# Kernel tuning notes

Hardware: AMD Instinct MI355X
Metric: run time of the kernel (lower is better)

The kernel has to match this reference:

```python
import jax, jax.numpy as jnp
import numpy as np

PAD_IDX = 1  # word2vec key_to_index['<PAD>'] / padding_idx in the original
VOCAB, EMBED, HIDDEN, SEQ = 100000, 300, 512, 1024


def setup_inputs() -> dict:
    key = jax.random.key(0)
    k = jax.random.split(key, 8)
    s = 1.0 / np.sqrt(HIDDEN)  # PyTorch LSTM init scale
    return {
        "input_seq": jax.random.randint(k[0], (1, SEQ), 0, VOCAB, dtype=jnp.int64)
                     if jax.config.jax_enable_x64 else
                     jax.random.randint(k[0], (1, SEQ), 0, VOCAB, dtype=jnp.int32),
        "h0": jnp.zeros((1, 1, HIDDEN), jnp.float32),
        "c0": jnp.zeros((1, 1, HIDDEN), jnp.float32),
        "emb": jax.random.normal(k[1], (VOCAB, EMBED), jnp.float32),  # frozen word2vec table
        "W_ih": jax.random.uniform(k[2], (4 * HIDDEN, EMBED), jnp.float32, -s, s),
        "W_hh": jax.random.uniform(k[3], (4 * HIDDEN, HIDDEN), jnp.float32, -s, s),
        "b_ih": jax.random.uniform(k[4], (4 * HIDDEN,), jnp.float32, -s, s),
        "b_hh": jax.random.uniform(k[5], (4 * HIDDEN,), jnp.float32, -s, s),
    }


def _lstm_scan(xs, is_pad, h, c, W_ih, W_hh, b_ih, b_hh):
    # xs: [S, E]; PAD steps leave (h, c, out) untouched, matching the `continue`.
    x_gates = xs @ W_ih.T + b_ih  # [S, 4H] -- hoist input projection out of the scan
    H = h.shape[-1]

    def step(carry, inp):
        h, c, out = carry
        xg, pad = inp
        g = xg + h @ W_hh.T + b_hh                 # [4H], PyTorch gate order i,f,g,o
        i, f, gg, o = jnp.split(g, 4)
        c_new = jax.nn.sigmoid(f) * c + jax.nn.sigmoid(i) * jnp.tanh(gg)
        h_new = jax.nn.sigmoid(o) * jnp.tanh(c_new)
        h = jnp.where(pad, h, h_new)
        c = jnp.where(pad, c, c_new)
        out = jnp.where(pad, out, h_new)
        return (h, c, out), None

    (h, c, out), _ = jax.lax.scan(step, (h, c, jnp.zeros(H, xs.dtype)), (x_gates, is_pad))
    return h, c, out


def reference(input_seq, h0, c0, emb, W_ih, W_hh, b_ih, b_hh):
    tokens = input_seq[0]                 # batch==1 in the original
    xs = emb[tokens]                      # [S, E] embedding gather (fused into recurrence)
    is_pad = tokens == PAD_IDX
    h, c, out = _lstm_scan(xs, is_pad, h0[0, 0], c0[0, 0], W_ih, W_hh, b_ih, b_hh)
    # original returns output=None if every token is PAD; here out stays zeros.
    return (out[None, None, :], (h[None, None, :], c[None, None, :]))
```

## Files before the change

### kernel.cpp

```cpp
#include <hip/hip_runtime.h>
#include <hip/hip_cooperative_groups.h>
#include <math.h>

#define SEQ    1024
#define EMBED  300
#define HIDDEN 512
#define G4     2048
#define NB     128
#define NBLK   256
#define TPB    256
#define UPB    (HIDDEN/NB)
#define PAD_IDX 1
#define SENT   0x7FC00BADu

#define HSLOT  32
#define HROW   (NB * HSLOT)

__device__ __align__(128) float g_xg[SEQ * G4];
__device__ __align__(128) float g_hp[(SEQ + 1) * HROW];
__device__ unsigned int g_done;
__device__ float        g_sink;

__device__ __forceinline__ float sigmoidf_(float x) {
    return 1.f / (1.f + __expf(-x));
}
__device__ __forceinline__ float tanhf_(float x) {
    return 1.f - 2.f / (__expf(2.f * x) + 1.f);
}

#define DPP_ADD(v, ctrl)                                                      \
    (v) += __int_as_float(__builtin_amdgcn_update_dpp(                        \
        0, __float_as_int(v), (ctrl), 0xf, 0xf, true))

#define LDA_U32(p) __hip_atomic_load((p), __ATOMIC_RELAXED, __HIP_MEMORY_SCOPE_AGENT)

__global__ __launch_bounds__(TPB, 1) void fused_kernel(
    const int* __restrict__ seq, const float* __restrict__ h0,
    const float* __restrict__ c0, const float* __restrict__ emb,
    const float* __restrict__ W_ih, const float* __restrict__ Whh,
    const float* __restrict__ b_ih, const float* __restrict__ b_hh,
    float* __restrict__ out)
{
    const int b = blockIdx.x, tid = threadIdx.x;
    const int gid = b * TPB + tid;

    if (gid == 0) g_done = 0u;
    for (int i = gid; i < (SEQ + 1) * HROW; i += NBLK * TPB) {
        int step = i >> 12, slot = i & (HROW - 1);
        int blk = slot >> 5, k = slot & (HSLOT - 1);
        float v = __uint_as_float(SENT);
        if (step == 0 && k < UPB) v = h0[blk * UPB + k];
        g_hp[i] = v;
    }
    for (int i = gid; i < SEQ * G4; i += NBLK * TPB)
        g_xg[i] = __uint_as_float(SENT);

    cooperative_groups::this_grid().sync();

    if (b >= NB) {
        const int hb = b - NB;
        __shared__ int tok_s[8];
        __shared__ __align__(16) float embt[8][304];

        for (int it = 0; it < 2; it++) {
            const int item  = hb + it * NB;
            const int t0    = (item >> 1) * 8;
            const int k_half = item & 1;

            if (tid < 8) tok_s[tid] = seq[t0 + tid];
            __syncthreads();
            for (int idx = tid; idx < 8 * EMBED; idx += TPB) {
                int tt = idx / EMBED;
                int e  = idx - tt * EMBED;
                embt[tt][e] = emb[(size_t)tok_s[tt] * EMBED + e];
            }
            __syncthreads();

            const int kbase = k_half * 1024 + tid;
            const float4* wr0 = (const float4*)(W_ih + (size_t)(kbase      ) * EMBED);
            const float4* wr1 = (const float4*)(W_ih + (size_t)(kbase + 256) * EMBED);
            const float4* wr2 = (const float4*)(W_ih + (size_t)(kbase + 512) * EMBED);
            const float4* wr3 = (const float4*)(W_ih + (size_t)(kbase + 768) * EMBED);

            float acc[4][8];
            #pragma unroll
            for (int kk = 0; kk < 4; kk++)
                #pragma unroll
                for (int tt = 0; tt < 8; tt++) acc[kk][tt] = 0.f;

            for (int e4 = 0; e4 < EMBED / 4; e4++) {
                float4 em[8];
                #pragma unroll
                for (int tt = 0; tt < 8; tt++)
                    em[tt] = *(const float4*)&embt[tt][e4 * 4];
                float4 w[4];
                w[0] = wr0[e4]; w[1] = wr1[e4]; w[2] = wr2[e4]; w[3] = wr3[e4];
                #pragma unroll
                for (int kk = 0; kk < 4; kk++) {
                    #pragma unroll
                    for (int tt = 0; tt < 8; tt++) {
                        float a = acc[kk][tt];
                        a = fmaf(w[kk].x, em[tt].x, a);
                        a = fmaf(w[kk].y, em[tt].y, a);
                        a = fmaf(w[kk].z, em[tt].z, a);
                        a = fmaf(w[kk].w, em[tt].w, a);
                        acc[kk][tt] = a;
                    }
                }
            }
            #pragma unroll
            for (int kk = 0; kk < 4; kk++) {
                int k = kbase + kk * 256;
                float bias = b_ih[k] + b_hh[k];
                #pragma unroll
                for (int tt = 0; tt < 8; tt++) {
                    __hip_atomic_store(&g_xg[(size_t)(t0 + tt) * G4 + k],
                                       acc[kk][tt] + bias,
                                       __ATOMIC_RELAXED, __HIP_MEMORY_SCOPE_AGENT);
                }
            }
            __syncthreads();
        }

        if (tid < 128) {
            float a0 = 1.0f + tid, a1 = 2.0f, a2 = 3.0f, a3 = 4.0f;
            for (;;) {
                #pragma unroll
                for (int i = 0; i < 128; i++) {
                    a0 = fmaf(a0, 1.000001f, 0.5f);
                    a1 = fmaf(a1, 0.999999f, 0.25f);
                    a2 = fmaf(a2, 1.0000005f, a0);
                    a3 = fmaf(a3, 0.9999995f, a1);
                }
                if (__hip_atomic_load(&g_done, __ATOMIC_RELAXED,
                                      __HIP_MEMORY_SCOPE_AGENT)) break;
            }
            if (a0 == 1234.5678f && a1 == a2) g_sink = a3;
        }
        return;
    }

    const int u = tid >> 6;
    const int lane = tid & 63;
    const int g = lane >> 4, c = lane & 15;
    const int R = g * HIDDEN + b * UPB + u;

    const float* wrow = Whh + (size_t)R * HIDDEN + c * 32;
    float4 wreg[8];
    #pragma unroll
    for (int i = 0; i < 8; i++) {
        int off = (4 * i + 4 * c) & 31;
        wreg[i] = *(const float4*)(wrow + off);
    }

    __shared__ __align__(16) float h_lds[2][HIDDEN];
    __shared__ int tok_lds[SEQ];

    for (int i = tid; i < SEQ; i += TPB) tok_lds[i] = seq[i];

    const bool owner = (lane == 0);
    const bool gate_lane = (c == 0);
    float c_state = 0.f, h_state = 0.f;
    if (owner) {
        c_state = c0[b * UPB + u];
        h_state = h0[b * UPB + u];
    }
    __syncthreads();

    int np = 0;
    bool any = false;

    for (int t = 0; t < SEQ; t++) {
        int tok = tok_lds[t];
        if (tok == PAD_IDX) continue;
        any = true;

        const unsigned* xgp = (const unsigned*)&g_xg[(size_t)t * G4
                                                     + g * HIDDEN + b * UPB + u];
        unsigned xgu = 0u;
        if (gate_lane) xgu = LDA_U32(xgp);

        if (tid < NB) {
            const unsigned long long* hb_ =
                (const unsigned long long*)(g_hp + (size_t)np * HROW + tid * HSLOT);
            unsigned long long p0, p1;
            for (;;) {
                p0 = __hip_atomic_load(hb_ + 0, __ATOMIC_RELAXED,
                                       __HIP_MEMORY_SCOPE_AGENT);
                p1 = __hip_atomic_load(hb_ + 1, __ATOMIC_RELAXED,
                                       __HIP_MEMORY_SCOPE_AGENT);
                if ((unsigned)p0 != SENT && (unsigned)(p0 >> 32) != SENT &&
                    (unsigned)p1 != SENT && (unsigned)(p1 >> 32) != SENT)
                    break;
            }
            unsigned long long* dst =
                (unsigned long long*)&h_lds[np & 1][tid * UPB];
            dst[0] = p0; dst[1] = p1;
        }
        __syncthreads();

        const float* hc = h_lds[np & 1] + c * 32;
        float4 a4 = {0.f, 0.f, 0.f, 0.f};
        #pragma unroll
        for (int i = 0; i < 8; i++) {
            int off = (4 * i + 4 * c) & 31;
            float4 h4 = *(const float4*)(hc + off);
            a4.x = fmaf(wreg[i].x, h4.x, a4.x);
            a4.y = fmaf(wreg[i].y, h4.y, a4.y);
            a4.z = fmaf(wreg[i].z, h4.z, a4.z);
            a4.w = fmaf(wreg[i].w, h4.w, a4.w);
        }
        float dotv = (a4.x + a4.y) + (a4.z + a4.w);
        DPP_ADD(dotv, 0xB1);
        DPP_ADD(dotv, 0x4E);
        DPP_ADD(dotv, 0x141);
        DPP_ADD(dotv, 0x140);

        float act = 0.f;
        if (gate_lane) {
            while (xgu == SENT) xgu = LDA_U32(xgp);
            float z = __uint_as_float(xgu) + dotv;
            act = (g == 2) ? tanhf_(z) : sigmoidf_(z);
        }
        float fv = __shfl(act, 16);
        float gv = __shfl(act, 32);
        float ov = __shfl(act, 48);

        if (owner) {
            c_state = fv * c_state + act * gv;
            h_state = ov * tanhf_(c_state);
            __hip_atomic_store(
                (unsigned*)(g_hp + (size_t)(np + 1) * HROW + b * HSLOT) + u,
                __float_as_uint(h_state),
                __ATOMIC_RELAXED, __HIP_MEMORY_SCOPE_AGENT);
        }
        np++;
    }

    if (owner) {
        int uo = b * UPB + u;
        out[uo]              = any ? h_state : 0.f;
        out[HIDDEN + uo]     = h_state;
        out[2 * HIDDEN + uo] = c_state;
    }
    if (b == 0 && tid == 0) {
        __hip_atomic_store(&g_done, 1u, __ATOMIC_RELAXED,
                           __HIP_MEMORY_SCOPE_AGENT);
    }
}

extern "C" void kernel_launch(void* const* d_in, const int* in_sizes, int n_in,
                              void* d_out, int out_size, void* d_ws, size_t ws_size,
                              hipStream_t stream)
{
    const int*   seq  = (const int*)  d_in[0];
    const float* h0   = (const float*)d_in[1];
    const float* c0   = (const float*)d_in[2];
    const float* emb  = (const float*)d_in[3];
    const float* W_ih = (const float*)d_in[4];
    const float* W_hh = (const float*)d_in[5];
    const float* b_ih = (const float*)d_in[6];
    const float* b_hh = (const float*)d_in[7];
    float* out = (float*)d_out;

    void* args[] = { (void*)&seq, (void*)&h0, (void*)&c0, (void*)&emb,
                     (void*)&W_ih, (void*)&W_hh, (void*)&b_ih, (void*)&b_hh,
                     (void*)&out };
    hipLaunchCooperativeKernel((const void*)fused_kernel, dim3(NBLK), dim3(TPB),
                               args, 0, stream);
}
```

Before: 1.937 ms.

## Fuse input projection into recurrent blocks and drop precomputed gate buffer

Removes the separate helper-block computation of x_gates and the global g_xg buffer. Each recurrent lane now keeps its slice of W_ih in registers, prefetches the next non-PAD token's embedding slice, and adds its partial input dot product into the existing DPP reduction. The h-broadcast buffer init now touches only the used slots instead of the whole padded array. This cuts the large sentinel fill and the cross-block polling on xg, at the cost of more registers and an embedding gather per step on the serial critical path.

```diff
diff --git a/kernel.cpp b/kernel.cpp
--- a/kernel.cpp
+++ b/kernel.cpp
@@ -5,7 +5,6 @@
 #define SEQ    1024
 #define EMBED  300
 #define HIDDEN 512
-#define G4     2048
 #define NB     128
 #define NBLK   256
 #define TPB    256
@@ -16,7 +15,6 @@
 #define HSLOT  32
 #define HROW   (NB * HSLOT)
 
-__device__ __align__(128) float g_xg[SEQ * G4];
 __device__ __align__(128) float g_hp[(SEQ + 1) * HROW];
 __device__ unsigned int g_done;
 __device__ float        g_sink;
@@ -31,8 +29,6 @@
 #define DPP_ADD(v, ctrl)                                                      \
     (v) += __int_as_float(__builtin_amdgcn_update_dpp(                        \
         0, __float_as_int(v), (ctrl), 0xf, 0xf, true))
-
-#define LDA_U32(p) __hip_atomic_load((p), __ATOMIC_RELAXED, __HIP_MEMORY_SCOPE_AGENT)
 
 __global__ __launch_bounds__(TPB, 1) void fused_kernel(
     const int* __restrict__ seq, const float* __restrict__ h0,
@@ -44,84 +40,19 @@
     const int b = blockIdx.x, tid = threadIdx.x;
     const int gid = b * TPB + tid;
 
+    for (int i = gid; i < (SEQ + 1) * NB * UPB; i += NBLK * TPB) {
+        int step = i >> 9;
+        int w    = i & 511;
+        int blk  = w >> 2, k = w & 3;
+        float v = __uint_as_float(SENT);
+        if (step == 0) v = h0[blk * UPB + k];
+        g_hp[(size_t)step * HROW + blk * HSLOT + k] = v;
+    }
     if (gid == 0) g_done = 0u;
-    for (int i = gid; i < (SEQ + 1) * HROW; i += NBLK * TPB) {
-        int step = i >> 12, slot = i & (HROW - 1);
-        int blk = slot >> 5, k = slot & (HSLOT - 1);
-        float v = __uint_as_float(SENT);
-        if (step == 0 && k < UPB) v = h0[blk * UPB + k];
-        g_hp[i] = v;
-    }
-    for (int i = gid; i < SEQ * G4; i += NBLK * TPB)
-        g_xg[i] = __uint_as_float(SENT);
 
     cooperative_groups::this_grid().sync();
 
     if (b >= NB) {
-        const int hb = b - NB;
-        __shared__ int tok_s[8];
-        __shared__ __align__(16) float embt[8][304];
-
-        for (int it = 0; it < 2; it++) {
-            const int item  = hb + it * NB;
-            const int t0    = (item >> 1) * 8;
-            const int k_half = item & 1;
-
-            if (tid < 8) tok_s[tid] = seq[t0 + tid];
-            __syncthreads();
-            for (int idx = tid; idx < 8 * EMBED; idx += TPB) {
-                int tt = idx / EMBED;
-                int e  = idx - tt * EMBED;
-                embt[tt][e] = emb[(size_t)tok_s[tt] * EMBED + e];
-            }
-            __syncthreads();
-
-            const int kbase = k_half * 1024 + tid;
-            const float4* wr0 = (const float4*)(W_ih + (size_t)(kbase      ) * EMBED);
-            const float4* wr1 = (const float4*)(W_ih + (size_t)(kbase + 256) * EMBED);
-            const float4* wr2 = (const float4*)(W_ih + (size_t)(kbase + 512) * EMBED);
-            const float4* wr3 = (const float4*)(W_ih + (size_t)(kbase + 768) * EMBED);
-
-            float acc[4][8];
-            #pragma unroll
-            for (int kk = 0; kk < 4; kk++)
-                #pragma unroll
-                for (int tt = 0; tt < 8; tt++) acc[kk][tt] = 0.f;
-
-            for (int e4 = 0; e4 < EMBED / 4; e4++) {
-                float4 em[8];
-                #pragma unroll
-                for (int tt = 0; tt < 8; tt++)
-                    em[tt] = *(const float4*)&embt[tt][e4 * 4];
-                float4 w[4];
-                w[0] = wr0[e4]; w[1] = wr1[e4]; w[2] = wr2[e4]; w[3] = wr3[e4];
-                #pragma unroll
-                for (int kk = 0; kk < 4; kk++) {
-                    #pragma unroll
-                    for (int tt = 0; tt < 8; tt++) {
-                        float a = acc[kk][tt];
-                        a = fmaf(w[kk].x, em[tt].x, a);
-                        a = fmaf(w[kk].y, em[tt].y, a);
-                        a = fmaf(w[kk].z, em[tt].z, a);
-                        a = fmaf(w[kk].w, em[tt].w, a);
-                        acc[kk][tt] = a;
-                    }
-                }
-            }
-            #pragma unroll
-            for (int kk = 0; kk < 4; kk++) {
-                int k = kbase + kk * 256;
-                float bias = b_ih[k] + b_hh[k];
-                #pragma unroll
-                for (int tt = 0; tt < 8; tt++) {
-                    __hip_atomic_store(&g_xg[(size_t)(t0 + tt) * G4 + k],
-                                       acc[kk][tt] + bias,
-                                       __ATOMIC_RELAXED, __HIP_MEMORY_SCOPE_AGENT);
-                }
-            }
-            __syncthreads();
-        }
-
         if (tid < 128) {
             float a0 = 1.0f + tid, a1 = 2.0f, a2 = 3.0f, a3 = 4.0f;
             for (;;) {
@@ -143,7 +74,8 @@
     const int u = tid >> 6;
     const int lane = tid & 63;
     const int g = lane >> 4, c = lane & 15;
-    const int R = g * HIDDEN + b * UPB + u;
+    const int U = b * UPB + u;
+    const int R = g * HIDDEN + U;
 
     const float* wrow = Whh + (size_t)R * HIDDEN + c * 32;
     float4 wreg[8];
@@ -153,19 +85,43 @@
         wreg[i] = *(const float4*)(wrow + off);
     }
 
+    float4 wih[5];
+    #pragma unroll
+    for (int j = 0; j < 5; j++) wih[j] = make_float4(0.f, 0.f, 0.f, 0.f);
+    if (c < 15) {
+        const float* xr = W_ih + (size_t)R * EMBED + c * 20;
+        #pragma unroll
+        for (int j = 0; j < 5; j++) wih[j] = *(const float4*)(xr + 4 * j);
+    }
+    const bool gate_lane = (c == 0);
+    float bias = 0.f;
+    if (gate_lane) bias = b_ih[R] + b_hh[R];
+
     __shared__ __align__(16) float h_lds[2][HIDDEN];
     __shared__ int tok_lds[SEQ];
 
     for (int i = tid; i < SEQ; i += TPB) tok_lds[i] = seq[i];
 
     const bool owner = (lane == 0);
-    const bool gate_lane = (c == 0);
     float c_state = 0.f, h_state = 0.f;
     if (owner) {
-        c_state = c0[b * UPB + u];
-        h_state = h0[b * UPB + u];
+        c_state = c0[U];
+        h_state = h0[U];
     }
     __syncthreads();
+
+    float4 er[5];
+    #pragma unroll
+    for (int j = 0; j < 5; j++) er[j] = make_float4(0.f, 0.f, 0.f, 0.f);
+    {
+        int tf = 0;
+        while (tf < SEQ && tok_lds[tf] == PAD_IDX) tf++;
+        if (tf < SEQ && c < 15) {
+            const float* ep = emb + (size_t)tok_lds[tf] * EMBED + c * 20;
+            #pragma unroll
+            for (int j = 0; j < 5; j++) er[j] = *(const float4*)(ep + 4 * j);
+        }
+    }
 
     int np = 0;
     bool any = false;
@@ -175,10 +131,21 @@
         if (tok == PAD_IDX) continue;
         any = true;
 
-        const unsigned* xgp = (const unsigned*)&g_xg[(size_t)t * G4
-                                                     + g * HIDDEN + b * UPB + u];
-        unsigned xgu = 0u;
-        if (gate_lane) xgu = LDA_U32(xgp);
+        float ix = 0.f;
+        #pragma unroll
+        for (int j = 0; j < 5; j++) {
+            ix = fmaf(wih[j].x, er[j].x, ix);
+            ix = fmaf(wih[j].y, er[j].y, ix);
+            ix = fmaf(wih[j].z, er[j].z, ix);
+            ix = fmaf(wih[j].w, er[j].w, ix);
+        }
+        int tn = t + 1;
+        while (tn < SEQ && tok_lds[tn] == PAD_IDX) tn++;
+        if (tn < SEQ && c < 15) {
+            const float* ep = emb + (size_t)tok_lds[tn] * EMBED + c * 20;
+            #pragma unroll
+            for (int j = 0; j < 5; j++) er[j] = *(const float4*)(ep + 4 * j);
+        }
 
         if (tid < NB) {
             const unsigned long long* hb_ =
@@ -210,7 +177,7 @@
             a4.z = fmaf(wreg[i].z, h4.z, a4.z);
             a4.w = fmaf(wreg[i].w, h4.w, a4.w);
         }
-        float dotv = (a4.x + a4.y) + (a4.z + a4.w);
+        float dotv = (a4.x + a4.y) + (a4.z + a4.w) + ix;
         DPP_ADD(dotv, 0xB1);
         DPP_ADD(dotv, 0x4E);
         DPP_ADD(dotv, 0x141);
@@ -218,8 +185,7 @@
 
         float act = 0.f;
         if (gate_lane) {
-            while (xgu == SENT) xgu = LDA_U32(xgp);
-            float z = __uint_as_float(xgu) + dotv;
+            float z = dotv + bias;
             act = (g == 2) ? tanhf_(z) : sigmoidf_(z);
         }
         float fv = __shfl(act, 16);
@@ -238,10 +204,9 @@
     }
 
     if (owner) {
-        int uo = b * UPB + u;
-        out[uo]              = any ? h_state : 0.f;
-        out[HIDDEN + uo]     = h_state;
-        out[2 * HIDDEN + uo] = c_state;
+        out[U]              = any ? h_state : 0.f;
+        out[HIDDEN + U]     = h_state;
+        out[2 * HIDDEN + U] = c_state;
     }
     if (b == 0 && tid == 0) {
         __hip_atomic_store(&g_done, 1u, __ATOMIC_RELAXED,
```

New measurement: 1.843 ms. -4.8%, faster.

## Shrink sentinel init and grid-sync input projection before recurrence

Applied to the files above, without the earlier changes.

Initialization of the h-exchange buffer now writes only the 4 used slots per block instead of all 32 padded slots, which cuts the global memory writes done before the first grid barrier. A second cooperative grid sync is added so the recurrent blocks start only after the helper blocks have finished the whole input projection. The per-step gate load then becomes a plain load, with a polling fallback kept only for the sentinel case. This trades the earlier overlap between the projection and the recurrence for cheaper per-step loads and less init traffic.

```diff
diff --git a/kernel.cpp b/kernel.cpp
--- a/kernel.cpp
+++ b/kernel.cpp
@@ -32,7 +32,8 @@
     (v) += __int_as_float(__builtin_amdgcn_update_dpp(                        \
         0, __float_as_int(v), (ctrl), 0xf, 0xf, true))
 
-#define LDA_U32(p) __hip_atomic_load((p), __ATOMIC_RELAXED, __HIP_MEMORY_SCOPE_AGENT)
+#define LDA(p)    __hip_atomic_load((p), __ATOMIC_RELAXED, __HIP_MEMORY_SCOPE_AGENT)
+#define STA(p, v) __hip_atomic_store((p), (v), __ATOMIC_RELAXED, __HIP_MEMORY_SCOPE_AGENT)
 
 __global__ __launch_bounds__(TPB, 1) void fused_kernel(
     const int* __restrict__ seq, const float* __restrict__ h0,
@@ -44,16 +45,17 @@
     const int b = blockIdx.x, tid = threadIdx.x;
     const int gid = b * TPB + tid;
 
+    for (int i = gid; i < (SEQ + 1) * NB * UPB; i += NBLK * TPB) {
+        int step = i >> 9;
+        int w    = i & 511;
+        int blk  = w >> 2, k = w & 3;
+        float v = __uint_as_float(SENT);
+        if (step == 0) v = h0[blk * UPB + k];
+        g_hp[(size_t)step * HROW + blk * HSLOT + k] = v;
+    }
+    for (int i = gid; i < SEQ * G4; i += NBLK * TPB)
+        STA((unsigned*)&g_xg[i], SENT);
     if (gid == 0) g_done = 0u;
-    for (int i = gid; i < (SEQ + 1) * HROW; i += NBLK * TPB) {
-        int step = i >> 12, slot = i & (HROW - 1);
-        int blk = slot >> 5, k = slot & (HSLOT - 1);
-        float v = __uint_as_float(SENT);
-        if (step == 0 && k < UPB) v = h0[blk * UPB + k];
-        g_hp[i] = v;
-    }
-    for (int i = gid; i < SEQ * G4; i += NBLK * TPB)
-        g_xg[i] = __uint_as_float(SENT);
 
     cooperative_groups::this_grid().sync();
 
@@ -63,8 +65,8 @@
         __shared__ __align__(16) float embt[8][304];
 
         for (int it = 0; it < 2; it++) {
-            const int item  = hb + it * NB;
-            const int t0    = (item >> 1) * 8;
+            const int item   = hb + it * NB;
+            const int t0     = (item >> 1) * 8;
             const int k_half = item & 1;
 
             if (tid < 8) tok_s[tid] = seq[t0 + tid];
@@ -114,13 +116,14 @@
                 float bias = b_ih[k] + b_hh[k];
                 #pragma unroll
                 for (int tt = 0; tt < 8; tt++) {
-                    __hip_atomic_store(&g_xg[(size_t)(t0 + tt) * G4 + k],
-                                       acc[kk][tt] + bias,
-                                       __ATOMIC_RELAXED, __HIP_MEMORY_SCOPE_AGENT);
+                    STA((unsigned*)&g_xg[(size_t)(t0 + tt) * G4 + k],
+                        __float_as_uint(acc[kk][tt] + bias));
                 }
             }
             __syncthreads();
         }
+
+        cooperative_groups::this_grid().sync();
 
         if (tid < 128) {
             float a0 = 1.0f + tid, a1 = 2.0f, a2 = 3.0f, a3 = 4.0f;
@@ -143,7 +146,8 @@
     const int u = tid >> 6;
     const int lane = tid & 63;
     const int g = lane >> 4, c = lane & 15;
-    const int R = g * HIDDEN + b * UPB + u;
+    const int U = b * UPB + u;
+    const int R = g * HIDDEN + U;
 
     const float* wrow = Whh + (size_t)R * HIDDEN + c * 32;
     float4 wreg[8];
@@ -162,10 +166,12 @@
     const bool gate_lane = (c == 0);
     float c_state = 0.f, h_state = 0.f;
     if (owner) {
-        c_state = c0[b * UPB + u];
-        h_state = h0[b * UPB + u];
+        c_state = c0[U];
+        h_state = h0[U];
     }
     __syncthreads();
+
+    cooperative_groups::this_grid().sync();
 
     int np = 0;
     bool any = false;
@@ -175,10 +181,10 @@
         if (tok == PAD_IDX) continue;
         any = true;
 
-        const unsigned* xgp = (const unsigned*)&g_xg[(size_t)t * G4
-                                                     + g * HIDDEN + b * UPB + u];
-        unsigned xgu = 0u;
-        if (gate_lane) xgu = LDA_U32(xgp);
+        const unsigned* xp = (const unsigned*)
+            &g_xg[(size_t)t * G4 + g * HIDDEN + U];
+        unsigned xv = 0u;
+        if (gate_lane) xv = *xp;
 
         if (tid < NB) {
             const unsigned long long* hb_ =
@@ -218,8 +224,8 @@
 
         float act = 0.f;
         if (gate_lane) {
-            while (xgu == SENT) xgu = LDA_U32(xgp);
-            float z = __uint_as_float(xgu) + dotv;
+            if (xv == SENT) { do { xv = LDA(xp); } while (xv == SENT); }
+            float z = __uint_as_float(xv) + dotv;
             act = (g == 2) ? tanhf_(z) : sigmoidf_(z);
         }
         float fv = __shfl(act, 16);
@@ -229,23 +235,19 @@
         if (owner) {
             c_state = fv * c_state + act * gv;
             h_state = ov * tanhf_(c_state);
-            __hip_atomic_store(
-                (unsigned*)(g_hp + (size_t)(np + 1) * HROW + b * HSLOT) + u,
-                __float_as_uint(h_state),
-                __ATOMIC_RELAXED, __HIP_MEMORY_SCOPE_AGENT);
+            STA((unsigned*)(g_hp + (size_t)(np + 1) * HROW + b * HSLOT) + u,
+                __float_as_uint(h_state));
         }
         np++;
     }
 
     if (owner) {
-        int uo = b * UPB + u;
-        out[uo]              = any ? h_state : 0.f;
-        out[HIDDEN + uo]     = h_state;
-        out[2 * HIDDEN + uo] = c_state;
+        out[U]              = any ? h_state : 0.f;
+        out[HIDDEN + U]     = h_state;
+        out[2 * HIDDEN + U] = c_state;
     }
     if (b == 0 && tid == 0) {
-        __hip_atomic_store(&g_done, 1u, __ATOMIC_RELAXED,
-                           __HIP_MEMORY_SCOPE_AGENT);
+        STA(&g_done, 1u);
     }
 }
 
```

After: 2.040 ms. 5.4% more time.
